# Kernel tuning notes

Measured on AMD Instinct MI355X. Metric: run time of the kernel, lower is better.

The kernel has to match this reference:

```python
import jax, jax.numpy as jnp
import numpy as np
import math

B, D, S, H = 4, 1024, 2048, 16


def setup_inputs() -> dict:
    key = jax.random.key(0)
    ks = jax.random.split(key, 9)
    scale = 0.02
    return {
        "x": jax.random.normal(ks[0], (B, D, S), dtype=jnp.float32),
        "Wq": jax.random.normal(ks[1], (D, D), dtype=jnp.float32) * scale,
        "bq": jnp.zeros((D,), dtype=jnp.float32),
        "Wk": jax.random.normal(ks[2], (D, D), dtype=jnp.float32) * scale,
        "bk": jnp.zeros((D,), dtype=jnp.float32),
        "Wv": jax.random.normal(ks[3], (D, D), dtype=jnp.float32) * scale,
        "bv": jnp.zeros((D,), dtype=jnp.float32),
        "Wo": jax.random.normal(ks[4], (D, D), dtype=jnp.float32) * scale,
        "bo": jnp.zeros((D,), dtype=jnp.float32),
        "num_heads": H,
    }


def _positional_encoding(d_model, seq_len):
    # pe[0::2, :] = sin(pos * denom), pe[1::2, :] = cos(pos * denom)
    pos = jnp.arange(seq_len, dtype=jnp.float32)[None, :]            # [1, S]
    denom = jnp.exp(jnp.arange(0, d_model, 2, dtype=jnp.float32)
                    * (-math.log(10000.0) / d_model))[:, None]        # [D/2, 1]
    angles = pos * denom                                              # [D/2, S]
    pe = jnp.zeros((d_model, seq_len), dtype=jnp.float32)
    pe = pe.at[0::2, :].set(jnp.sin(angles))
    pe = pe.at[1::2, :].set(jnp.cos(angles))
    return pe


def reference(x, Wq, bq, Wk, bk, Wv, bv, Wo, bo, num_heads):
    b, d_model, s = x.shape
    head_dim = d_model // num_heads
    x = x + _positional_encoding(d_model, s)[None, :, :]  # broadcast over batch
    x = jnp.transpose(x, (0, 2, 1))                       # [B, S, D]
    q = x @ Wq.T + bq
    k = x @ Wk.T + bk
    v = x @ Wv.T + bv
    # [B, S, H, hd] -> [B, H, S, hd]
    q = q.reshape(b, s, num_heads, head_dim).transpose(0, 2, 1, 3)
    k = k.reshape(b, s, num_heads, head_dim).transpose(0, 2, 1, 3)
    v = v.reshape(b, s, num_heads, head_dim).transpose(0, 2, 1, 3)
    scores = jnp.einsum('bhqd,bhkd->bhqk', q, k) / jnp.sqrt(
        jnp.asarray(head_dim, dtype=jnp.float32))
    attn = jax.nn.softmax(scores, axis=-1)
    out = jnp.einsum('bhqk,bhkd->bhqd', attn, v)          # [B, H, S, hd]
    out = out.transpose(0, 2, 1, 3).reshape(b, s, d_model)
    out = out @ Wo.T + bo
    return jnp.transpose(out, (0, 2, 1))                  # [B, D, S]
```

## Files before the change

### kernel.cpp

```cpp
#include <hip/hip_runtime.h>


typedef __bf16 bf16;
typedef __attribute__((ext_vector_type(8))) __bf16 bf16x8;
typedef __attribute__((ext_vector_type(4))) __bf16 bf16x4;
typedef __attribute__((ext_vector_type(2))) __bf16 bf16x2;
typedef __attribute__((ext_vector_type(4))) float f32x4;
typedef __attribute__((ext_vector_type(2))) unsigned int uintx2;
typedef __attribute__((ext_vector_type(4))) unsigned int uintx4;

#define NB 4
#define ND 1024
#define NS 2048
#define NH 16
#define NM 8192

__device__ __forceinline__ void gld16(const void* g, void* l) {
  __builtin_amdgcn_global_load_lds((__attribute__((address_space(1))) void*)g,
                                   (__attribute__((address_space(3))) void*)l, 16, 0, 0);
}

__device__ __forceinline__ float exp2_fast(float x) {
#if __has_builtin(__builtin_amdgcn_exp2f)
  return __builtin_amdgcn_exp2f(x);
#else
  return exp2f(x);
#endif
}

__device__ __forceinline__ unsigned pk2(float a, float b) {
  bf16x2 t;
  t[0] = (bf16)a;
  t[1] = (bf16)b;
  return __builtin_bit_cast(unsigned int, t);
}

__device__ __forceinline__ void lane_xchg(unsigned a, unsigned b, unsigned& lo,
                                          unsigned& hi) {
#if __has_builtin(__builtin_amdgcn_permlane32_swap) && \
    __has_builtin(__builtin_amdgcn_permlane16_swap)
  uintx2 r = __builtin_amdgcn_permlane32_swap(a, b, false, false);
  uintx2 r2 = __builtin_amdgcn_permlane16_swap(r[0], r[1], false, false);
  lo = r2[0];
  hi = r2[1];
#else
  const int lane = threadIdx.x & 63;
  const int src = (lane & 15) + ((lane >> 4) & 1) * 32;
  const unsigned as = (unsigned)__shfl((int)a, src, 64);
  const unsigned bs = (unsigned)__shfl((int)b, src, 64);
  const unsigned as2 = (unsigned)__shfl((int)a, src + 16, 64);
  const unsigned bs2 = (unsigned)__shfl((int)b, src + 16, 64);
  lo = (lane >= 32) ? bs : as;
  hi = (lane >= 32) ? bs2 : as2;
#endif
}

__global__ __launch_bounds__(256) void prep_x_kernel(const float* __restrict__ x,
                                                     bf16* __restrict__ xT) {
  __shared__ float t[32][33];
  const int tx = threadIdx.x, ty = threadIdx.y;
  const int s0 = blockIdx.x * 32, d0 = blockIdx.y * 32, b = blockIdx.z;
#pragma unroll
  for (int i = 0; i < 4; ++i) {
    const int rr = ty + i * 8;
    const int d = d0 + rr, s = s0 + tx;
    const float freq = __expf(-(float)(d >> 1) * 0.01798894603980689f);
    const float ang = (float)s * freq;
    const float pe = (d & 1) ? cosf(ang) : sinf(ang);
    t[rr][tx] = x[((size_t)b * ND + d) * NS + s] + pe;
  }
  __syncthreads();
#pragma unroll
  for (int i = 0; i < 4; ++i) {
    const int a = ty + i * 8;
    xT[((size_t)b * NS + s0 + a) * ND + d0 + tx] = (bf16)t[tx][a];
  }
}

__global__ __launch_bounds__(256) void prep_w_kernel(const float* __restrict__ Wq,
                                                     const float* __restrict__ Wk,
                                                     const float* __restrict__ Wv,
                                                     const float* __restrict__ Wo,
                                                     bf16* __restrict__ Wqkv,
                                                     bf16* __restrict__ WoB) {
  const size_t t = (size_t)blockIdx.x * blockDim.x + threadIdx.x;
  const size_t i = t * 4;
  const float* src;
  bf16* dst;
  size_t off;
  if (i < (size_t)3 * 1024 * 1024) {
    const int sel = (int)(i >> 20);
    src = sel == 0 ? Wq : (sel == 1 ? Wk : Wv);
    off = i - ((size_t)sel << 20);
    dst = Wqkv + i;
  } else {
    src = Wo;
    off = i - ((size_t)3 << 20);
    dst = WoB + off;
  }
  const f32x4 v = *(const f32x4*)(src + off);
  bf16x4 o;
  o[0] = (bf16)v[0];
  o[1] = (bf16)v[1];
  o[2] = (bf16)v[2];
  o[3] = (bf16)v[3];
  *(bf16x4*)dst = o;
}

__device__ __forceinline__ void gemm_tile_128(const bf16* __restrict__ A,
                                              const bf16* __restrict__ Bm,
                                              int tm, int tn, bf16* ldsA, bf16* ldsB,
                                              f32x4 acc[4][4]) {
  const int tid = threadIdx.x;
  const int lane = tid & 63, wave = tid >> 6;
  const int wm = wave >> 1, wn = wave & 1;
  const int rl = lane & 15, quad = lane >> 4;
  int r0[4], c0[4];
#pragma unroll
  for (int j = 0; j < 4; ++j) {
    const int o = (wave * 4 + j) * 1024 + lane * 16;
    const int r = o >> 7;
    r0[j] = r;
    c0[j] = ((((o >> 4) & 7) ^ (r & 7)) * 8);
  }
  for (int kt = 0; kt < 1024; kt += 64) {
#pragma unroll
    for (int j = 0; j < 4; ++j) {
      gld16(A + (size_t)(tm + r0[j]) * 1024 + kt + c0[j], (char*)ldsA + (wave * 4 + j) * 1024);
      gld16(Bm + (size_t)(tn + r0[j]) * 1024 + kt + c0[j], (char*)ldsB + (wave * 4 + j) * 1024);
    }
    __syncthreads();
#pragma unroll
    for (int kk = 0; kk < 2; ++kk) {
      bf16x8 af[4], bfr[4];
#pragma unroll
      for (int i = 0; i < 4; ++i) {
        const int ra = wm * 64 + i * 16 + rl;
        af[i] = *(const bf16x8*)((const char*)ldsA + ra * 128 +
                                 (((kk * 4 + quad) ^ (rl & 7)) * 16));
        const int rb = wn * 64 + i * 16 + rl;
        bfr[i] = *(const bf16x8*)((const char*)ldsB + rb * 128 +
                                  (((kk * 4 + quad) ^ (rl & 7)) * 16));
      }
#pragma unroll
      for (int i = 0; i < 4; ++i)
#pragma unroll
        for (int j = 0; j < 4; ++j)
          acc[i][j] =
              __builtin_amdgcn_mfma_f32_16x16x32_bf16(af[i], bfr[j], acc[i][j], 0, 0, 0);
    }
    __syncthreads();
  }
}

__global__ __launch_bounds__(256, 2) void gemm_qkv_kernel(
    const bf16* __restrict__ xT, const bf16* __restrict__ Wqkv,
    const float* __restrict__ bq, const float* __restrict__ bk,
    const float* __restrict__ bv, bf16* __restrict__ Q, bf16* __restrict__ Kb,
    bf16* __restrict__ VT) {
  __shared__ bf16 ldsA[128 * 64], ldsB[128 * 64];
  const int tm = blockIdx.x * 128, tn = blockIdx.y * 128;
  f32x4 acc[4][4];
  const f32x4 z = {0.f, 0.f, 0.f, 0.f};
#pragma unroll
  for (int i = 0; i < 4; ++i)
#pragma unroll
    for (int j = 0; j < 4; ++j) acc[i][j] = z;
  gemm_tile_128(xT, Wqkv, tm, tn, ldsA, ldsB, acc);
  const int lane = threadIdx.x & 63, wave = threadIdx.x >> 6;
  const int wm = wave >> 1, wn = wave & 1;
  const int rl = lane & 15, quad = lane >> 4;
  const float QSCALE = 0.18033688011112042f;
#pragma unroll
  for (int j = 0; j < 4; ++j) {
    const int n = tn + wn * 64 + j * 16 + rl;
    const int which = n >> 10;
    const int nl = n & 1023;
    const int h = nl >> 6, d = nl & 63;
    const float bias = (which == 0 ? bq : which == 1 ? bk : bv)[nl];
#pragma unroll
    for (int i = 0; i < 4; ++i) {
      const int m0 = tm + wm * 64 + i * 16 + quad * 4;
      const int b = m0 >> 11, s0 = m0 & 2047;
      const size_t bh = (size_t)(b * 16 + h);
      if (which == 2) {
        bf16x4 pk;
#pragma unroll
        for (int r = 0; r < 4; ++r) pk[r] = (bf16)(acc[i][j][r] + bias);
        *(bf16x4*)(VT + ((size_t)bh * 64 + d) * 2048 + s0) = pk;
      } else {
#pragma unroll
        for (int r = 0; r < 4; ++r) {
          const float v = acc[i][j][r] + bias;
          const int s = s0 + r;
          if (which == 0)
            Q[(bh * 2048 + s) * 64 + d] = (bf16)(v * QSCALE);
          else
            Kb[(bh * 2048 + s) * 64 + d] = (bf16)v;
        }
      }
    }
  }
}

__global__ __launch_bounds__(256, 4) void attn_kernel(const bf16* __restrict__ Q,
                                                      const bf16* __restrict__ Kb,
                                                      const bf16* __restrict__ VT,
                                                      bf16* __restrict__ AO) {
  __shared__ __align__(16) char smem[32768];
  char* ldsK = smem;
  char* ldsV = smem + 16384;
  const int tid = threadIdx.x;
  const int lane = tid & 63, wave = tid >> 6;
  const int rl = lane & 15, quad = lane >> 4;
  const int bh = blockIdx.x;
  const int q0 = blockIdx.y * 128;
  const bf16* Qb = Q + ((size_t)bh * 2048 + q0) * 64;
  const bf16* Kbb = Kb + (size_t)bh * 2048 * 64;
  const bf16* Vb = VT + (size_t)bh * 64 * 2048;
  const int o0 = wave * 1024 + lane * 16, o1 = o0 + 4096;
  const int ra = o0 >> 7, rb = o1 >> 7;
  const int ca = (((o0 >> 4) & 7) ^ (ra & 7)) * 16;
  const int cb = (((o1 >> 4) & 7) ^ (rb & 7)) * 16;
  gld16((const char*)Kbb + (size_t)ra * 128 + ca, ldsK + wave * 1024);
  gld16((const char*)Kbb + (size_t)rb * 128 + cb, ldsK + wave * 1024 + 4096);
  gld16((const char*)Vb + (size_t)ra * 4096 + ca, ldsV + wave * 1024);
  gld16((const char*)Vb + (size_t)rb * 4096 + cb, ldsV + wave * 1024 + 4096);
  bf16x8 qf[2][2];
#pragma unroll
  for (int i = 0; i < 2; ++i)
#pragma unroll
    for (int ks = 0; ks < 2; ++ks)
      qf[i][ks] =
          *(const bf16x8*)(Qb + (wave * 32 + i * 16 + rl) * 64 + ks * 32 + quad * 8);
  f32x4 o_acc[2][4], lacc[2];
  const f32x4 z = {0.f, 0.f, 0.f, 0.f};
#pragma unroll
  for (int i = 0; i < 2; ++i) {
    lacc[i] = z;
#pragma unroll
    for (int j = 0; j < 4; ++j) o_acc[i][j] = z;
  }
  const bf16 oneb = (bf16)1.0f;
  const bf16x8 onesb = {oneb, oneb, oneb, oneb, oneb, oneb, oneb, oneb};
  int buf = 0;
  for (int kt = 0; kt < 2048; kt += 64, buf ^= 1) {
    __syncthreads();
    if (kt + 64 < 2048) {
      const int nb = (buf ^ 1) * 8192;
      gld16((const char*)Kbb + (size_t)(kt + 64 + ra) * 128 + ca, ldsK + nb + wave * 1024);
      gld16((const char*)Kbb + (size_t)(kt + 64 + rb) * 128 + cb,
            ldsK + nb + wave * 1024 + 4096);
      gld16((const char*)Vb + (size_t)ra * 4096 + (size_t)(kt + 64) * 2 + ca,
            ldsV + nb + wave * 1024);
      gld16((const char*)Vb + (size_t)rb * 4096 + (size_t)(kt + 64) * 2 + cb,
            ldsV + nb + wave * 1024 + 4096);
    }
    const char* Kbase = ldsK + buf * 8192;
    const char* Vbase = ldsV + buf * 8192;
#pragma unroll
    for (int ks = 0; ks < 2; ++ks) {
      const int jk0 = ks * 2, jk1 = ks * 2 + 1;
      const bf16x8 k00 =
          *(const bf16x8*)(Kbase + (jk0 * 16 + rl) * 128 + ((quad ^ (rl & 7)) * 16));
      const bf16x8 k01 =
          *(const bf16x8*)(Kbase + (jk0 * 16 + rl) * 128 + (((4 + quad) ^ (rl & 7)) * 16));
      const bf16x8 k10 =
          *(const bf16x8*)(Kbase + (jk1 * 16 + rl) * 128 + ((quad ^ (rl & 7)) * 16));
      const bf16x8 k11 =
          *(const bf16x8*)(Kbase + (jk1 * 16 + rl) * 128 + (((4 + quad) ^ (rl & 7)) * 16));
      bf16x8 pf[2];
#pragma unroll
      for (int i = 0; i < 2; ++i) {
        f32x4 s0 = z, s1 = z;
        s0 = __builtin_amdgcn_mfma_f32_16x16x32_bf16(k00, qf[i][0], s0, 0, 0, 0);
        s0 = __builtin_amdgcn_mfma_f32_16x16x32_bf16(k01, qf[i][1], s0, 0, 0, 0);
        s1 = __builtin_amdgcn_mfma_f32_16x16x32_bf16(k10, qf[i][0], s1, 0, 0, 0);
        s1 = __builtin_amdgcn_mfma_f32_16x16x32_bf16(k11, qf[i][1], s1, 0, 0, 0);
        const unsigned a0 = pk2(exp2_fast(s0[0]), exp2_fast(s0[1]));
        const unsigned a1 = pk2(exp2_fast(s0[2]), exp2_fast(s0[3]));
        const unsigned b0 = pk2(exp2_fast(s1[0]), exp2_fast(s1[1]));
        const unsigned b1 = pk2(exp2_fast(s1[2]), exp2_fast(s1[3]));
        unsigned d0, d1, d2, d3;
        lane_xchg(a0, b0, d0, d2);
        lane_xchg(a1, b1, d1, d3);
        uintx4 dd;
        dd[0] = d0;
        dd[1] = d1;
        dd[2] = d2;
        dd[3] = d3;
        pf[i] = __builtin_bit_cast(bf16x8, dd);
        lacc[i] =
            __builtin_amdgcn_mfma_f32_16x16x32_bf16(pf[i], onesb, lacc[i], 0, 0, 0);
      }
#pragma unroll
      for (int j = 0; j < 4; ++j) {
        const bf16x8 vf = *(const bf16x8*)(Vbase + (j * 16 + rl) * 128 +
                                           (((ks * 4 + quad) ^ (rl & 7)) * 16));
#pragma unroll
        for (int i = 0; i < 2; ++i)
          o_acc[i][j] =
              __builtin_amdgcn_mfma_f32_16x16x32_bf16(pf[i], vf, o_acc[i][j], 0, 0, 0);
      }
    }
  }
  const int b = bh >> 4, h = bh & 15;
#pragma unroll
  for (int i = 0; i < 2; ++i) {
    f32x4 linv;
#pragma unroll
    for (int r = 0; r < 4; ++r) linv[r] = __builtin_amdgcn_rcpf(lacc[i][r]);
#pragma unroll
    for (int j = 0; j < 4; ++j)
#pragma unroll
      for (int r = 0; r < 4; ++r) {
        const int s = q0 + wave * 32 + i * 16 + quad * 4 + r;
        const int d = h * 64 + j * 16 + rl;
        AO[((size_t)b * 2048 + s) * 1024 + d] = (bf16)(o_acc[i][j][r] * linv[r]);
      }
  }
}

__global__ __launch_bounds__(256, 2) void gemm_out_kernel(const bf16* __restrict__ AO,
                                                          const bf16* __restrict__ WoB,
                                                          const float* __restrict__ bo,
                                                          float* __restrict__ out) {
  __shared__ bf16 ldsA[128 * 64], ldsB[128 * 64];
  const int tm = blockIdx.x * 128, tn = blockIdx.y * 128;
  f32x4 acc[4][4];
  const f32x4 z = {0.f, 0.f, 0.f, 0.f};
#pragma unroll
  for (int i = 0; i < 4; ++i)
#pragma unroll
    for (int j = 0; j < 4; ++j) acc[i][j] = z;
  gemm_tile_128(AO, WoB, tm, tn, ldsA, ldsB, acc);
  const int lane = threadIdx.x & 63, wave = threadIdx.x >> 6;
  const int wm = wave >> 1, wn = wave & 1;
  const int rl = lane & 15, quad = lane >> 4;
#pragma unroll
  for (int j = 0; j < 4; ++j) {
    const int n = tn + wn * 64 + j * 16 + rl;
    const float bias = bo[n];
#pragma unroll
    for (int i = 0; i < 4; ++i) {
      const int m0 = tm + wm * 64 + i * 16 + quad * 4;
      const int b = m0 >> 11, s = m0 & 2047;
      f32x4 v = acc[i][j];
      v[0] += bias;
      v[1] += bias;
      v[2] += bias;
      v[3] += bias;
      *(f32x4*)(out + ((size_t)(b * 1024 + n)) * 2048 + s) = v;
    }
  }
}

extern "C" void kernel_launch(void* const* d_in, const int* in_sizes, int n_in,
                              void* d_out, int out_size, void* d_ws, size_t ws_size,
                              hipStream_t stream) {
  const float* x = (const float*)d_in[0];
  const float* Wq = (const float*)d_in[1];
  const float* bq = (const float*)d_in[2];
  const float* Wk = (const float*)d_in[3];
  const float* bk = (const float*)d_in[4];
  const float* Wv = (const float*)d_in[5];
  const float* bv = (const float*)d_in[6];
  const float* Wo = (const float*)d_in[7];
  const float* bo = (const float*)d_in[8];
  float* out = (float*)d_out;

  char* p = (char*)d_ws;
  bf16* xT = (bf16*)p;
  p += (size_t)NM * ND * 2;
  bf16* Wqkv = (bf16*)p;
  p += (size_t)3 * ND * ND * 2;
  bf16* WoB = (bf16*)p;
  p += (size_t)ND * ND * 2;
  bf16* Qb = (bf16*)p;
  p += (size_t)NM * ND * 2;
  bf16* Kbf = (bf16*)p;
  p += (size_t)NM * ND * 2;
  bf16* VTb = (bf16*)p;
  p += (size_t)NM * ND * 2;
  bf16* AO = xT;

  prep_x_kernel<<<dim3(NS / 32, ND / 32, NB), dim3(32, 8), 0, stream>>>(x, xT);
  prep_w_kernel<<<dim3(4096), dim3(256), 0, stream>>>(Wq, Wk, Wv, Wo, Wqkv, WoB);
  gemm_qkv_kernel<<<dim3(NM / 128, 3072 / 128), dim3(256), 0, stream>>>(
      xT, Wqkv, bq, bk, bv, Qb, Kbf, VTb);
  attn_kernel<<<dim3(NB * NH, NS / 128), dim3(256), 0, stream>>>(Qb, Kbf, VTb, AO);
  gemm_out_kernel<<<dim3(NM / 128, ND / 128), dim3(256), 0, stream>>>(AO, WoB, bo, out);
}
```

Before: 266.5 us.

## Stagger K-slice order per wave, hoist LDS offsets, raise priority around MFMA bursts

After: 262.3 us. No clear change (-1.6%).

```diff
diff --git a/kernel.cpp b/kernel.cpp
--- a/kernel.cpp
+++ b/kernel.cpp
@@ -243,6 +243,16 @@
   }
   const bf16 oneb = (bf16)1.0f;
   const bf16x8 onesb = {oneb, oneb, oneb, oneb, oneb, oneb, oneb, oneb};
+  const int kcol0 = (quad ^ (rl & 7)) * 16 + rl * 128;
+  const int kcol1 = ((4 + quad) ^ (rl & 7)) * 16 + rl * 128;
+  const int ksr = wave & 1;
+  int ksOff[2], vcol[2];
+#pragma unroll
+  for (int ksi = 0; ksi < 2; ++ksi) {
+    const int ks = ksi ^ ksr;
+    ksOff[ksi] = ks * 4096;
+    vcol[ksi] = ((ks * 4 + quad) ^ (rl & 7)) * 16 + rl * 128;
+  }
   int buf = 0;
   for (int kt = 0; kt < 2048; kt += 64, buf ^= 1) {
     __syncthreads();
@@ -259,28 +269,31 @@
     const char* Kbase = ldsK + buf * 8192;
     const char* Vbase = ldsV + buf * 8192;
 #pragma unroll
-    for (int ks = 0; ks < 2; ++ks) {
-      const int jk0 = ks * 2, jk1 = ks * 2 + 1;
-      const bf16x8 k00 =
-          *(const bf16x8*)(Kbase + (jk0 * 16 + rl) * 128 + ((quad ^ (rl & 7)) * 16));
-      const bf16x8 k01 =
-          *(const bf16x8*)(Kbase + (jk0 * 16 + rl) * 128 + (((4 + quad) ^ (rl & 7)) * 16));
-      const bf16x8 k10 =
-          *(const bf16x8*)(Kbase + (jk1 * 16 + rl) * 128 + ((quad ^ (rl & 7)) * 16));
-      const bf16x8 k11 =
-          *(const bf16x8*)(Kbase + (jk1 * 16 + rl) * 128 + (((4 + quad) ^ (rl & 7)) * 16));
-      bf16x8 pf[2];
+    for (int ksi = 0; ksi < 2; ++ksi) {
+      const bf16x8 k00 = *(const bf16x8*)(Kbase + ksOff[ksi] + kcol0);
+      const bf16x8 k01 = *(const bf16x8*)(Kbase + ksOff[ksi] + kcol1);
+      const bf16x8 k10 = *(const bf16x8*)(Kbase + ksOff[ksi] + 2048 + kcol0);
+      const bf16x8 k11 = *(const bf16x8*)(Kbase + ksOff[ksi] + 2048 + kcol1);
+      f32x4 s[2][2];
+      __builtin_amdgcn_s_setprio(1);
 #pragma unroll
       for (int i = 0; i < 2; ++i) {
-        f32x4 s0 = z, s1 = z;
-        s0 = __builtin_amdgcn_mfma_f32_16x16x32_bf16(k00, qf[i][0], s0, 0, 0, 0);
-        s0 = __builtin_amdgcn_mfma_f32_16x16x32_bf16(k01, qf[i][1], s0, 0, 0, 0);
-        s1 = __builtin_amdgcn_mfma_f32_16x16x32_bf16(k10, qf[i][0], s1, 0, 0, 0);
-        s1 = __builtin_amdgcn_mfma_f32_16x16x32_bf16(k11, qf[i][1], s1, 0, 0, 0);
-        const unsigned a0 = pk2(exp2_fast(s0[0]), exp2_fast(s0[1]));
-        const unsigned a1 = pk2(exp2_fast(s0[2]), exp2_fast(s0[3]));
-        const unsigned b0 = pk2(exp2_fast(s1[0]), exp2_fast(s1[1]));
-        const unsigned b1 = pk2(exp2_fast(s1[2]), exp2_fast(s1[3]));
+        s[i][0] = __builtin_amdgcn_mfma_f32_16x16x32_bf16(k00, qf[i][0], z, 0, 0, 0);
+        s[i][0] = __builtin_amdgcn_mfma_f32_16x16x32_bf16(k01, qf[i][1], s[i][0], 0, 0, 0);
+        s[i][1] = __builtin_amdgcn_mfma_f32_16x16x32_bf16(k10, qf[i][0], z, 0, 0, 0);
+        s[i][1] = __builtin_amdgcn_mfma_f32_16x16x32_bf16(k11, qf[i][1], s[i][1], 0, 0, 0);
+      }
+      __builtin_amdgcn_s_setprio(0);
+      bf16x8 vf[4];
+#pragma unroll
+      for (int j = 0; j < 4; ++j)
+        vf[j] = *(const bf16x8*)(Vbase + j * 2048 + vcol[ksi]);
+#pragma unroll
+      for (int i = 0; i < 2; ++i) {
+        const unsigned a0 = pk2(exp2_fast(s[i][0][0]), exp2_fast(s[i][0][1]));
+        const unsigned a1 = pk2(exp2_fast(s[i][0][2]), exp2_fast(s[i][0][3]));
+        const unsigned b0 = pk2(exp2_fast(s[i][1][0]), exp2_fast(s[i][1][1]));
+        const unsigned b1 = pk2(exp2_fast(s[i][1][2]), exp2_fast(s[i][1][3]));
         unsigned d0, d1, d2, d3;
         lane_xchg(a0, b0, d0, d2);
         lane_xchg(a1, b1, d1, d3);
@@ -289,18 +302,15 @@
         dd[1] = d1;
         dd[2] = d2;
         dd[3] = d3;
-        pf[i] = __builtin_bit_cast(bf16x8, dd);
+        const bf16x8 pf = __builtin_bit_cast(bf16x8, dd);
+        __builtin_amdgcn_s_setprio(1);
         lacc[i] =
-            __builtin_amdgcn_mfma_f32_16x16x32_bf16(pf[i], onesb, lacc[i], 0, 0, 0);
-      }
-#pragma unroll
-      for (int j = 0; j < 4; ++j) {
-        const bf16x8 vf = *(const bf16x8*)(Vbase + (j * 16 + rl) * 128 +
-                                           (((ks * 4 + quad) ^ (rl & 7)) * 16));
-#pragma unroll
-        for (int i = 0; i < 2; ++i)
+            __builtin_amdgcn_mfma_f32_16x16x32_bf16(pf, onesb, lacc[i], 0, 0, 0);
+#pragma unroll
+        for (int j = 0; j < 4; ++j)
           o_acc[i][j] =
-              __builtin_amdgcn_mfma_f32_16x16x32_bf16(pf[i], vf, o_acc[i][j], 0, 0, 0);
+              __builtin_amdgcn_mfma_f32_16x16x32_bf16(pf, vf[j], o_acc[i][j], 0, 0, 0);
+        __builtin_amdgcn_s_setprio(0);
       }
     }
   }
```

## Load K/V fragments directly from global memory in attention, drop LDS staging

Applied to the files above, without the earlier changes.

After: 421.4 us. 1.58x slower.

```diff
diff --git a/kernel.cpp b/kernel.cpp
--- a/kernel.cpp
+++ b/kernel.cpp
@@ -207,32 +207,20 @@
                                                       const bf16* __restrict__ Kb,
                                                       const bf16* __restrict__ VT,
                                                       bf16* __restrict__ AO) {
-  __shared__ __align__(16) char smem[32768];
-  char* ldsK = smem;
-  char* ldsV = smem + 16384;
   const int tid = threadIdx.x;
   const int lane = tid & 63, wave = tid >> 6;
   const int rl = lane & 15, quad = lane >> 4;
   const int bh = blockIdx.x;
-  const int q0 = blockIdx.y * 128;
+  const int q0 = blockIdx.y * 128 + wave * 32;
   const bf16* Qb = Q + ((size_t)bh * 2048 + q0) * 64;
-  const bf16* Kbb = Kb + (size_t)bh * 2048 * 64;
-  const bf16* Vb = VT + (size_t)bh * 64 * 2048;
-  const int o0 = wave * 1024 + lane * 16, o1 = o0 + 4096;
-  const int ra = o0 >> 7, rb = o1 >> 7;
-  const int ca = (((o0 >> 4) & 7) ^ (ra & 7)) * 16;
-  const int cb = (((o1 >> 4) & 7) ^ (rb & 7)) * 16;
-  gld16((const char*)Kbb + (size_t)ra * 128 + ca, ldsK + wave * 1024);
-  gld16((const char*)Kbb + (size_t)rb * 128 + cb, ldsK + wave * 1024 + 4096);
-  gld16((const char*)Vb + (size_t)ra * 4096 + ca, ldsV + wave * 1024);
-  gld16((const char*)Vb + (size_t)rb * 4096 + cb, ldsV + wave * 1024 + 4096);
+  const bf16* kbase = Kb + ((size_t)bh * 2048 + rl) * 64 + quad * 8;
+  const bf16* vbase = VT + ((size_t)bh * 64 + rl) * 2048 + quad * 8;
   bf16x8 qf[2][2];
 #pragma unroll
   for (int i = 0; i < 2; ++i)
 #pragma unroll
     for (int ks = 0; ks < 2; ++ks)
-      qf[i][ks] =
-          *(const bf16x8*)(Qb + (wave * 32 + i * 16 + rl) * 64 + ks * 32 + quad * 8);
+      qf[i][ks] = *(const bf16x8*)(Qb + (i * 16 + rl) * 64 + ks * 32 + quad * 8);
   f32x4 o_acc[2][4], lacc[2];
   const f32x4 z = {0.f, 0.f, 0.f, 0.f};
 #pragma unroll
@@ -243,40 +231,26 @@
   }
   const bf16 oneb = (bf16)1.0f;
   const bf16x8 onesb = {oneb, oneb, oneb, oneb, oneb, oneb, oneb, oneb};
-  int buf = 0;
-  for (int kt = 0; kt < 2048; kt += 64, buf ^= 1) {
-    __syncthreads();
-    if (kt + 64 < 2048) {
-      const int nb = (buf ^ 1) * 8192;
-      gld16((const char*)Kbb + (size_t)(kt + 64 + ra) * 128 + ca, ldsK + nb + wave * 1024);
-      gld16((const char*)Kbb + (size_t)(kt + 64 + rb) * 128 + cb,
-            ldsK + nb + wave * 1024 + 4096);
-      gld16((const char*)Vb + (size_t)ra * 4096 + (size_t)(kt + 64) * 2 + ca,
-            ldsV + nb + wave * 1024);
-      gld16((const char*)Vb + (size_t)rb * 4096 + (size_t)(kt + 64) * 2 + cb,
-            ldsV + nb + wave * 1024 + 4096);
-    }
-    const char* Kbase = ldsK + buf * 8192;
-    const char* Vbase = ldsV + buf * 8192;
+  for (int kt = 0; kt < 2048; kt += 64) {
 #pragma unroll
     for (int ks = 0; ks < 2; ++ks) {
-      const int jk0 = ks * 2, jk1 = ks * 2 + 1;
-      const bf16x8 k00 =
-          *(const bf16x8*)(Kbase + (jk0 * 16 + rl) * 128 + ((quad ^ (rl & 7)) * 16));
-      const bf16x8 k01 =
-          *(const bf16x8*)(Kbase + (jk0 * 16 + rl) * 128 + (((4 + quad) ^ (rl & 7)) * 16));
-      const bf16x8 k10 =
-          *(const bf16x8*)(Kbase + (jk1 * 16 + rl) * 128 + ((quad ^ (rl & 7)) * 16));
-      const bf16x8 k11 =
-          *(const bf16x8*)(Kbase + (jk1 * 16 + rl) * 128 + (((4 + quad) ^ (rl & 7)) * 16));
-      bf16x8 pf[2];
+      const int krow = kt + ks * 32;
+      const bf16x8 k00 = *(const bf16x8*)(kbase + (size_t)krow * 64);
+      const bf16x8 k01 = *(const bf16x8*)(kbase + (size_t)krow * 64 + 32);
+      const bf16x8 k10 = *(const bf16x8*)(kbase + (size_t)(krow + 16) * 64);
+      const bf16x8 k11 = *(const bf16x8*)(kbase + (size_t)(krow + 16) * 64 + 32);
+      bf16x8 vf[4];
+#pragma unroll
+      for (int j = 0; j < 4; ++j)
+        vf[j] = *(const bf16x8*)(vbase + (size_t)(j * 16) * 2048 + krow);
 #pragma unroll
       for (int i = 0; i < 2; ++i) {
-        f32x4 s0 = z, s1 = z;
-        s0 = __builtin_amdgcn_mfma_f32_16x16x32_bf16(k00, qf[i][0], s0, 0, 0, 0);
+        __builtin_amdgcn_s_setprio(1);
+        f32x4 s0 = __builtin_amdgcn_mfma_f32_16x16x32_bf16(k00, qf[i][0], z, 0, 0, 0);
         s0 = __builtin_amdgcn_mfma_f32_16x16x32_bf16(k01, qf[i][1], s0, 0, 0, 0);
-        s1 = __builtin_amdgcn_mfma_f32_16x16x32_bf16(k10, qf[i][0], s1, 0, 0, 0);
+        f32x4 s1 = __builtin_amdgcn_mfma_f32_16x16x32_bf16(k10, qf[i][0], z, 0, 0, 0);
         s1 = __builtin_amdgcn_mfma_f32_16x16x32_bf16(k11, qf[i][1], s1, 0, 0, 0);
+        __builtin_amdgcn_s_setprio(0);
         const unsigned a0 = pk2(exp2_fast(s0[0]), exp2_fast(s0[1]));
         const unsigned a1 = pk2(exp2_fast(s0[2]), exp2_fast(s0[3]));
         const unsigned b0 = pk2(exp2_fast(s1[0]), exp2_fast(s1[1]));
@@ -289,18 +263,14 @@
         dd[1] = d1;
         dd[2] = d2;
         dd[3] = d3;
-        pf[i] = __builtin_bit_cast(bf16x8, dd);
-        lacc[i] =
-            __builtin_amdgcn_mfma_f32_16x16x32_bf16(pf[i], onesb, lacc[i], 0, 0, 0);
-      }
-#pragma unroll
-      for (int j = 0; j < 4; ++j) {
-        const bf16x8 vf = *(const bf16x8*)(Vbase + (j * 16 + rl) * 128 +
-                                           (((ks * 4 + quad) ^ (rl & 7)) * 16));
-#pragma unroll
-        for (int i = 0; i < 2; ++i)
+        const bf16x8 pf = __builtin_bit_cast(bf16x8, dd);
+        __builtin_amdgcn_s_setprio(1);
+        lacc[i] = __builtin_amdgcn_mfma_f32_16x16x32_bf16(pf, onesb, lacc[i], 0, 0, 0);
+#pragma unroll
+        for (int j = 0; j < 4; ++j)
           o_acc[i][j] =
-              __builtin_amdgcn_mfma_f32_16x16x32_bf16(pf[i], vf, o_acc[i][j], 0, 0, 0);
+              __builtin_amdgcn_mfma_f32_16x16x32_bf16(pf, vf[j], o_acc[i][j], 0, 0, 0);
+        __builtin_amdgcn_s_setprio(0);
       }
     }
   }
@@ -314,7 +284,7 @@
     for (int j = 0; j < 4; ++j)
 #pragma unroll
       for (int r = 0; r < 4; ++r) {
-        const int s = q0 + wave * 32 + i * 16 + quad * 4 + r;
+        const int s = q0 + i * 16 + quad * 4 + r;
         const int d = h * 64 + j * 16 + rl;
         AO[((size_t)b * 2048 + s) * 1024 + d] = (bf16)(o_acc[i][j][r] * linv[r]);
       }
```
